# Kernel optimization log

Hardware: AMD Instinct MI355X
Metric: run time of the kernel (lower is better)

## Reference

```python
import jax, jax.numpy as jnp
import numpy as np

B, H = 65536, 256  # batch, hidden_size (== input_size since combine = input + hidden)


def setup_inputs() -> dict:
    key = jax.random.key(0)
    ks = jax.random.split(key, 11)
    s = 1.0 / np.sqrt(H)  # nn.Linear default init scale
    return {
        "input": jax.random.normal(ks[0], (B, H), jnp.float32),
        "hidden": jax.random.normal(ks[1], (B, H), jnp.float32),
        "cell": jax.random.normal(ks[2], (B, H), jnp.float32),
        "Wf": jax.random.uniform(ks[3], (H, H), jnp.float32, -s, s),
        "bf": jax.random.uniform(ks[4], (H,), jnp.float32, -s, s),
        "Wc": jax.random.uniform(ks[5], (H, H), jnp.float32, -s, s),
        "bc": jax.random.uniform(ks[6], (H,), jnp.float32, -s, s),
        "Wi": jax.random.uniform(ks[7], (H, H), jnp.float32, -s, s),
        "bi": jax.random.uniform(ks[8], (H,), jnp.float32, -s, s),
        "Wo": jax.random.uniform(ks[9], (H, H), jnp.float32, -s, s),
        "bo": jax.random.uniform(ks[10], (H,), jnp.float32, -s, s),
    }


def reference(input, hidden, cell, Wf, bf, Wc, bc, Wi, bi, Wo, bo):
    combine = input + hidden                                   # [B, H]
    ft = jax.nn.sigmoid(combine @ Wf.T + bf)                   # forget gate
    ct_ = jnp.tanh(combine @ Wc.T + bc)                        # candidate
    it = jax.nn.sigmoid(jax.nn.sigmoid(combine @ Wi.T + bi))   # note: double sigmoid, as in source
    cell_state = cell * ft + ct_ * it                          # [B, H]
    out = jax.nn.sigmoid(combine @ Wo.T + bo)                  # output gate
    hidden_state = out * jnp.tanh(cell_state)
    return (out, hidden_state, cell_state)
```

## Files before the change

kernel.cpp:

```cpp
#include <hip/hip_runtime.h>
#include <hip/hip_bf16.h>


typedef __attribute__((ext_vector_type(8))) short short8;
typedef __attribute__((ext_vector_type(4))) float f32x4;

static constexpr int Bsz   = 65536;
static constexpr int Hdim  = 256;
static constexpr int TROWS = 64;
static constexpr int NBLK  = (Bsz / TROWS) * 2;

__device__ __forceinline__ short f2bf(float f) {
    unsigned u = __float_as_uint(f);
    return (short)((u + 0x7FFFu + ((u >> 16) & 1u)) >> 16);
}
__device__ __forceinline__ float fast_rcp(float x) {
    float r;
    asm("v_rcp_f32 %0, %1" : "=v"(r) : "v"(x));
    return r;
}
__device__ __forceinline__ float sigm(float x) {
    return fast_rcp(1.0f + __expf(-x));
}
__device__ __forceinline__ float tanh_fast(float x) {
    return 2.0f * fast_rcp(1.0f + __expf(-2.0f * x)) - 1.0f;
}

__global__ void __launch_bounds__(256)
prep_w_kernel(const float* __restrict__ Wf, const float* __restrict__ Wc,
              const float* __restrict__ Wi, const float* __restrict__ Wo,
              short* __restrict__ Bp)
{
    int o    = blockIdx.x * 256 + threadIdx.x;
    int e    = o & 7;
    int lane = (o >> 3) & 63;
    int jf   = (o >> 9) & 15;
    int ks   = (o >> 13) & 7;
    int g    = (o >> 16) & 3;
    int k = ks * 32 + (lane >> 4) * 8 + e;
    int j = jf * 16 + (lane & 15);
    const float* W = (g == 0) ? Wf : (g == 1) ? Wc : (g == 2) ? Wi : Wo;
    Bp[o] = f2bf(W[j * 256 + k]);
}

__global__ void __launch_bounds__(512, 4)
lstm_main(const float* __restrict__ inp, const float* __restrict__ hid,
          const float* __restrict__ cell, const short* __restrict__ Bp,
          const float* __restrict__ bfv, const float* __restrict__ bcv,
          const float* __restrict__ biv, const float* __restrict__ bov,
          float* __restrict__ out)
{
    __shared__ short As[TROWS * Hdim];

    const int tid  = threadIdx.x;
    const int lane = tid & 63;
    const int wave = tid >> 6;
    const int lm   = lane & 15;
    const int lk   = lane >> 4;

    const int bid     = blockIdx.x;
    const int rowtile = (bid >> 4) * 8 + (bid & 7);
    const int jh      = (bid >> 3) & 1;
    const int rowblk  = rowtile * TROWS;

    const int j         = jh * 128 + wave * 16 + lm;
    const int jf_global = jh * 8 + wave;

#pragma unroll
    for (int round = 0; round < 2; ++round) {
        float4 Li[2][2], Lh[2][2];
#pragma unroll
        for (int c = 0; c < 2; ++c) {
            int cc  = tid + (round * 2 + c) * 512;
            int row = cc >> 5;
            int k0  = (cc & 31) * 8;
            const float4* ip = reinterpret_cast<const float4*>(inp + (size_t)(rowblk + row) * Hdim + k0);
            const float4* hp = reinterpret_cast<const float4*>(hid + (size_t)(rowblk + row) * Hdim + k0);
            Li[c][0] = ip[0]; Li[c][1] = ip[1];
            Lh[c][0] = hp[0]; Lh[c][1] = hp[1];
        }
#pragma unroll
        for (int c = 0; c < 2; ++c) {
            int cc  = tid + (round * 2 + c) * 512;
            int row = cc >> 5;
            int k0  = (cc & 31) * 8;
            short8 v;
            v[0] = f2bf(Li[c][0].x + Lh[c][0].x);
            v[1] = f2bf(Li[c][0].y + Lh[c][0].y);
            v[2] = f2bf(Li[c][0].z + Lh[c][0].z);
            v[3] = f2bf(Li[c][0].w + Lh[c][0].w);
            v[4] = f2bf(Li[c][1].x + Lh[c][1].x);
            v[5] = f2bf(Li[c][1].y + Lh[c][1].y);
            v[6] = f2bf(Li[c][1].z + Lh[c][1].z);
            v[7] = f2bf(Li[c][1].w + Lh[c][1].w);
            int byte = (row * 512 + k0 * 2) ^ ((row & 7) << 4);
            *reinterpret_cast<short8*>(reinterpret_cast<char*>(As) + byte) = v;
        }
    }

    const float bF = bfv[j], bC = bcv[j], bI = biv[j], bO = bov[j];

    __syncthreads();

    f32x4 acc[4][4];
    acc[0][0] = (f32x4){bF, bF, bF, bF};
    acc[1][0] = (f32x4){bC, bC, bC, bC};
    acc[2][0] = (f32x4){bI, bI, bI, bI};
    acc[3][0] = (f32x4){bO, bO, bO, bO};
#pragma unroll
    for (int g = 0; g < 4; ++g)
#pragma unroll
        for (int mf = 1; mf < 4; ++mf)
            acc[g][mf] = acc[g][0];

    const char* A = reinterpret_cast<const char*>(As);
#pragma unroll
    for (int ks = 0; ks < 8; ++ks) {
        short8 cf[4];
#pragma unroll
        for (int mf = 0; mf < 4; ++mf) {
            int row  = mf * 16 + lm;
            int byte = (row * 512 + (ks * 32 + lk * 8) * 2) ^ ((row & 7) << 4);
            cf[mf] = *reinterpret_cast<const short8*>(A + byte);
        }
#pragma unroll
        for (int g = 0; g < 4; ++g) {
            int chunk = (g * 8 + ks) * 16 + jf_global;
            short8 b = *reinterpret_cast<const short8*>(
                           Bp + ((size_t)chunk * 64 + lane) * 8);
            acc[g][0] = __builtin_amdgcn_mfma_f32_16x16x32_bf16(cf[0], b, acc[g][0], 0, 0, 0);
            acc[g][1] = __builtin_amdgcn_mfma_f32_16x16x32_bf16(cf[1], b, acc[g][1], 0, 0, 0);
            acc[g][2] = __builtin_amdgcn_mfma_f32_16x16x32_bf16(cf[2], b, acc[g][2], 0, 0, 0);
            acc[g][3] = __builtin_amdgcn_mfma_f32_16x16x32_bf16(cf[3], b, acc[g][3], 0, 0, 0);
        }
    }

    float* out0 = out;
    float* out1 = out + (size_t)Bsz * Hdim;
    float* out2 = out + (size_t)2 * Bsz * Hdim;

#pragma unroll
    for (int mf = 0; mf < 4; ++mf) {
        float cv[4];
#pragma unroll
        for (int r = 0; r < 4; ++r)
            cv[r] = cell[(size_t)(rowblk + mf * 16 + lk * 4 + r) * Hdim + j];
#pragma unroll
        for (int r = 0; r < 4; ++r) {
            int row = rowblk + mf * 16 + lk * 4 + r;
            size_t off = (size_t)row * Hdim + j;
            float F = sigm(acc[0][mf][r]);
            float C = tanh_fast(acc[1][mf][r]);
            float I = sigm(sigm(acc[2][mf][r]));
            float O = sigm(acc[3][mf][r]);
            float cs = cv[r] * F + C * I;
            float hs = O * tanh_fast(cs);
            out0[off] = O;
            out1[off] = hs;
            out2[off] = cs;
        }
    }
}

extern "C" void kernel_launch(void* const* d_in, const int* in_sizes, int n_in,
                              void* d_out, int out_size, void* d_ws, size_t ws_size,
                              hipStream_t stream)
{
    const float* inp  = (const float*)d_in[0];
    const float* hid  = (const float*)d_in[1];
    const float* cell = (const float*)d_in[2];
    const float* Wf   = (const float*)d_in[3];
    const float* bf_  = (const float*)d_in[4];
    const float* Wc   = (const float*)d_in[5];
    const float* bc_  = (const float*)d_in[6];
    const float* Wi   = (const float*)d_in[7];
    const float* bi_  = (const float*)d_in[8];
    const float* Wo   = (const float*)d_in[9];
    const float* bo_  = (const float*)d_in[10];

    short* Bp = (short*)d_ws;

    prep_w_kernel<<<1024, 256, 0, stream>>>(Wf, Wc, Wi, Wo, Bp);
    lstm_main<<<NBLK, 512, 0, stream>>>(inp, hid, cell, Bp,
                                        bf_, bc_, bi_, bo_, (float*)d_out);
}
```

Baseline: 116.2 us.

## Process two row tiles per block, prefetching second tile during first MFMA loop

Each block now handles two 64-row tiles using a double-buffered LDS staging area. Loads of the second tile's input and hidden rows are issued before the first tile's MFMA k-loop, so global-load latency overlaps with compute. The grid is halved and the occupancy hint drops from 4 to 2 blocks per CU. LDS use doubles and more registers hold the prefetched data, which may lower occupancy.

```diff
diff --git a/kernel.cpp b/kernel.cpp
--- a/kernel.cpp
+++ b/kernel.cpp
@@ -8,7 +8,7 @@
 static constexpr int Bsz   = 65536;
 static constexpr int Hdim  = 256;
 static constexpr int TROWS = 64;
-static constexpr int NBLK  = (Bsz / TROWS) * 2;
+static constexpr int NBLK  = (Bsz / (TROWS * 2)) * 2;
 
 __device__ __forceinline__ short f2bf(float f) {
     unsigned u = __float_as_uint(f);
@@ -43,14 +43,14 @@
     Bp[o] = f2bf(W[j * 256 + k]);
 }
 
-__global__ void __launch_bounds__(512, 4)
+__global__ void __launch_bounds__(512, 2)
 lstm_main(const float* __restrict__ inp, const float* __restrict__ hid,
           const float* __restrict__ cell, const short* __restrict__ Bp,
           const float* __restrict__ bfv, const float* __restrict__ bcv,
           const float* __restrict__ biv, const float* __restrict__ bov,
           float* __restrict__ out)
 {
-    __shared__ short As[TROWS * Hdim];
+    __shared__ short As[2][TROWS * Hdim];
 
     const int tid  = threadIdx.x;
     const int lane = tid & 63;
@@ -59,31 +59,34 @@
     const int lk   = lane >> 4;
 
     const int bid     = blockIdx.x;
-    const int rowtile = (bid >> 4) * 8 + (bid & 7);
+    const int rowpair = (bid >> 4) * 8 + (bid & 7);
     const int jh      = (bid >> 3) & 1;
-    const int rowblk  = rowtile * TROWS;
+    const int rowblk  = rowpair * (TROWS * 2);
 
     const int j         = jh * 128 + wave * 16 + lm;
     const int jf_global = jh * 8 + wave;
 
-#pragma unroll
-    for (int round = 0; round < 2; ++round) {
-        float4 Li[2][2], Lh[2][2];
-#pragma unroll
-        for (int c = 0; c < 2; ++c) {
-            int cc  = tid + (round * 2 + c) * 512;
-            int row = cc >> 5;
-            int k0  = (cc & 31) * 8;
-            const float4* ip = reinterpret_cast<const float4*>(inp + (size_t)(rowblk + row) * Hdim + k0);
-            const float4* hp = reinterpret_cast<const float4*>(hid + (size_t)(rowblk + row) * Hdim + k0);
+    const int s_row = tid >> 5;
+    const int s_k0  = (tid & 31) * 8;
+
+    float4 Li[4][2], Lh[4][2];
+
+    auto issue = [&](int t) {
+#pragma unroll
+        for (int c = 0; c < 4; ++c) {
+            int row = s_row + c * 16;
+            const float4* ip = reinterpret_cast<const float4*>(
+                inp + (size_t)(rowblk + t * TROWS + row) * Hdim + s_k0);
+            const float4* hp = reinterpret_cast<const float4*>(
+                hid + (size_t)(rowblk + t * TROWS + row) * Hdim + s_k0);
             Li[c][0] = ip[0]; Li[c][1] = ip[1];
             Lh[c][0] = hp[0]; Lh[c][1] = hp[1];
         }
-#pragma unroll
-        for (int c = 0; c < 2; ++c) {
-            int cc  = tid + (round * 2 + c) * 512;
-            int row = cc >> 5;
-            int k0  = (cc & 31) * 8;
+    };
+    auto writeb = [&](int buf) {
+#pragma unroll
+        for (int c = 0; c < 4; ++c) {
+            int row = s_row + c * 16;
             short8 v;
             v[0] = f2bf(Li[c][0].x + Lh[c][0].x);
             v[1] = f2bf(Li[c][0].y + Lh[c][0].y);
@@ -93,73 +96,93 @@
             v[5] = f2bf(Li[c][1].y + Lh[c][1].y);
             v[6] = f2bf(Li[c][1].z + Lh[c][1].z);
             v[7] = f2bf(Li[c][1].w + Lh[c][1].w);
-            int byte = (row * 512 + k0 * 2) ^ ((row & 7) << 4);
-            *reinterpret_cast<short8*>(reinterpret_cast<char*>(As) + byte) = v;
-        }
-    }
+            int byte = (row * 512 + s_k0 * 2) ^ ((row & 7) << 4);
+            *reinterpret_cast<short8*>(
+                reinterpret_cast<char*>(As[buf]) + byte) = v;
+        }
+    };
 
     const float bF = bfv[j], bC = bcv[j], bI = biv[j], bO = bov[j];
 
-    __syncthreads();
-
-    f32x4 acc[4][4];
-    acc[0][0] = (f32x4){bF, bF, bF, bF};
-    acc[1][0] = (f32x4){bC, bC, bC, bC};
-    acc[2][0] = (f32x4){bI, bI, bI, bI};
-    acc[3][0] = (f32x4){bO, bO, bO, bO};
-#pragma unroll
-    for (int g = 0; g < 4; ++g)
-#pragma unroll
-        for (int mf = 1; mf < 4; ++mf)
-            acc[g][mf] = acc[g][0];
-
-    const char* A = reinterpret_cast<const char*>(As);
-#pragma unroll
-    for (int ks = 0; ks < 8; ++ks) {
-        short8 cf[4];
-#pragma unroll
-        for (int mf = 0; mf < 4; ++mf) {
-            int row  = mf * 16 + lm;
-            int byte = (row * 512 + (ks * 32 + lk * 8) * 2) ^ ((row & 7) << 4);
-            cf[mf] = *reinterpret_cast<const short8*>(A + byte);
-        }
-#pragma unroll
-        for (int g = 0; g < 4; ++g) {
-            int chunk = (g * 8 + ks) * 16 + jf_global;
-            short8 b = *reinterpret_cast<const short8*>(
-                           Bp + ((size_t)chunk * 64 + lane) * 8);
-            acc[g][0] = __builtin_amdgcn_mfma_f32_16x16x32_bf16(cf[0], b, acc[g][0], 0, 0, 0);
-            acc[g][1] = __builtin_amdgcn_mfma_f32_16x16x32_bf16(cf[1], b, acc[g][1], 0, 0, 0);
-            acc[g][2] = __builtin_amdgcn_mfma_f32_16x16x32_bf16(cf[2], b, acc[g][2], 0, 0, 0);
-            acc[g][3] = __builtin_amdgcn_mfma_f32_16x16x32_bf16(cf[3], b, acc[g][3], 0, 0, 0);
-        }
-    }
+    auto kloop = [&](const short* Abuf, f32x4 (&acc)[4][4]) {
+        acc[0][0] = (f32x4){bF, bF, bF, bF};
+        acc[1][0] = (f32x4){bC, bC, bC, bC};
+        acc[2][0] = (f32x4){bI, bI, bI, bI};
+        acc[3][0] = (f32x4){bO, bO, bO, bO};
+#pragma unroll
+        for (int g = 0; g < 4; ++g)
+#pragma unroll
+            for (int mf = 1; mf < 4; ++mf)
+                acc[g][mf] = acc[g][0];
+        const char* A = reinterpret_cast<const char*>(Abuf);
+#pragma unroll
+        for (int ks = 0; ks < 8; ++ks) {
+            short8 cf[4];
+#pragma unroll
+            for (int mf = 0; mf < 4; ++mf) {
+                int row  = mf * 16 + lm;
+                int byte = (row * 512 + (ks * 32 + lk * 8) * 2) ^ ((row & 7) << 4);
+                cf[mf] = *reinterpret_cast<const short8*>(A + byte);
+            }
+#pragma unroll
+            for (int g = 0; g < 4; ++g) {
+                int chunk = (g * 8 + ks) * 16 + jf_global;
+                short8 b = *reinterpret_cast<const short8*>(
+                               Bp + ((size_t)chunk * 64 + lane) * 8);
+                acc[g][0] = __builtin_amdgcn_mfma_f32_16x16x32_bf16(cf[0], b, acc[g][0], 0, 0, 0);
+                acc[g][1] = __builtin_amdgcn_mfma_f32_16x16x32_bf16(cf[1], b, acc[g][1], 0, 0, 0);
+                acc[g][2] = __builtin_amdgcn_mfma_f32_16x16x32_bf16(cf[2], b, acc[g][2], 0, 0, 0);
+                acc[g][3] = __builtin_amdgcn_mfma_f32_16x16x32_bf16(cf[3], b, acc[g][3], 0, 0, 0);
+            }
+        }
+    };
 
     float* out0 = out;
     float* out1 = out + (size_t)Bsz * Hdim;
     float* out2 = out + (size_t)2 * Bsz * Hdim;
 
-#pragma unroll
-    for (int mf = 0; mf < 4; ++mf) {
-        float cv[4];
-#pragma unroll
-        for (int r = 0; r < 4; ++r)
-            cv[r] = cell[(size_t)(rowblk + mf * 16 + lk * 4 + r) * Hdim + j];
-#pragma unroll
-        for (int r = 0; r < 4; ++r) {
-            int row = rowblk + mf * 16 + lk * 4 + r;
-            size_t off = (size_t)row * Hdim + j;
-            float F = sigm(acc[0][mf][r]);
-            float C = tanh_fast(acc[1][mf][r]);
-            float I = sigm(sigm(acc[2][mf][r]));
-            float O = sigm(acc[3][mf][r]);
-            float cs = cv[r] * F + C * I;
-            float hs = O * tanh_fast(cs);
-            out0[off] = O;
-            out1[off] = hs;
-            out2[off] = cs;
-        }
-    }
+    auto epilogue = [&](int t, f32x4 (&acc)[4][4]) {
+        const int r0 = rowblk + t * TROWS;
+#pragma unroll
+        for (int mf = 0; mf < 4; ++mf) {
+            float cv[4];
+#pragma unroll
+            for (int r = 0; r < 4; ++r)
+                cv[r] = cell[(size_t)(r0 + mf * 16 + lk * 4 + r) * Hdim + j];
+#pragma unroll
+            for (int r = 0; r < 4; ++r) {
+                int row = r0 + mf * 16 + lk * 4 + r;
+                size_t off = (size_t)row * Hdim + j;
+                float F = sigm(acc[0][mf][r]);
+                float C = tanh_fast(acc[1][mf][r]);
+                float I = sigm(sigm(acc[2][mf][r]));
+                float O = sigm(acc[3][mf][r]);
+                float cs = cv[r] * F + C * I;
+                float hs = O * tanh_fast(cs);
+                out0[off] = O;
+                out1[off] = hs;
+                out2[off] = cs;
+            }
+        }
+    };
+
+    issue(0);
+    asm volatile("" ::: "memory");
+    writeb(0);
+    __syncthreads();
+
+    issue(1);
+    asm volatile("" ::: "memory");
+
+    f32x4 acc[4][4];
+    kloop(As[0], acc);
+
+    writeb(1);
+    __syncthreads();
+
+    epilogue(0, acc);
+    kloop(As[1], acc);
+    epilogue(1, acc);
 }
 
 extern "C" void kernel_launch(void* const* d_in, const int* in_sizes, int n_in,
```

New measurement: 152.5 us. 31.2% more time.

## Process two row tiles per block, overlapping next tile loads with epilogue

Applied to the files above, without the earlier changes.

Each block now handles two 64-row tiles with double-buffered LDS, which halves the grid size. Global loads of input and hidden for the second tile are issued before the first tile's epilogue, so memory latency is hidden behind the activation math and stores. The cost is doubled LDS per block (64KB), which may reduce occupancy, plus higher register pressure from keeping loads in flight during the epilogue.

```diff
diff --git a/kernel.cpp b/kernel.cpp
--- a/kernel.cpp
+++ b/kernel.cpp
@@ -8,7 +8,7 @@
 static constexpr int Bsz   = 65536;
 static constexpr int Hdim  = 256;
 static constexpr int TROWS = 64;
-static constexpr int NBLK  = (Bsz / TROWS) * 2;
+static constexpr int NBLK  = (Bsz / (TROWS * 2)) * 2;
 
 __device__ __forceinline__ short f2bf(float f) {
     unsigned u = __float_as_uint(f);
@@ -50,7 +50,7 @@
           const float* __restrict__ biv, const float* __restrict__ bov,
           float* __restrict__ out)
 {
-    __shared__ short As[TROWS * Hdim];
+    __shared__ short As[2][TROWS * Hdim];
 
     const int tid  = threadIdx.x;
     const int lane = tid & 63;
@@ -59,26 +59,36 @@
     const int lk   = lane >> 4;
 
     const int bid     = blockIdx.x;
-    const int rowtile = (bid >> 4) * 8 + (bid & 7);
+    const int rowpair = (bid >> 4) * 8 + (bid & 7);
     const int jh      = (bid >> 3) & 1;
-    const int rowblk  = rowtile * TROWS;
+    const int rowblk  = rowpair * (TROWS * 2);
 
     const int j         = jh * 128 + wave * 16 + lm;
     const int jf_global = jh * 8 + wave;
 
-#pragma unroll
-    for (int round = 0; round < 2; ++round) {
-        float4 Li[2][2], Lh[2][2];
+    float* out0 = out;
+    float* out1 = out + (size_t)Bsz * Hdim;
+    float* out2 = out + (size_t)2 * Bsz * Hdim;
+
+    const float bF = bfv[j], bC = bcv[j], bI = biv[j], bO = bov[j];
+
+    f32x4 acc[4][4];
+
+    auto issue_round = [&](int t, int round, float4 (&Li)[2][2], float4 (&Lh)[2][2]) {
 #pragma unroll
         for (int c = 0; c < 2; ++c) {
             int cc  = tid + (round * 2 + c) * 512;
             int row = cc >> 5;
             int k0  = (cc & 31) * 8;
-            const float4* ip = reinterpret_cast<const float4*>(inp + (size_t)(rowblk + row) * Hdim + k0);
-            const float4* hp = reinterpret_cast<const float4*>(hid + (size_t)(rowblk + row) * Hdim + k0);
+            const float4* ip = reinterpret_cast<const float4*>(
+                inp + (size_t)(rowblk + t * TROWS + row) * Hdim + k0);
+            const float4* hp = reinterpret_cast<const float4*>(
+                hid + (size_t)(rowblk + t * TROWS + row) * Hdim + k0);
             Li[c][0] = ip[0]; Li[c][1] = ip[1];
             Lh[c][0] = hp[0]; Lh[c][1] = hp[1];
         }
+    };
+    auto write_round = [&](int buf, int round, float4 (&Li)[2][2], float4 (&Lh)[2][2]) {
 #pragma unroll
         for (int c = 0; c < 2; ++c) {
             int cc  = tid + (round * 2 + c) * 512;
@@ -94,72 +104,96 @@
             v[6] = f2bf(Li[c][1].z + Lh[c][1].z);
             v[7] = f2bf(Li[c][1].w + Lh[c][1].w);
             int byte = (row * 512 + k0 * 2) ^ ((row & 7) << 4);
-            *reinterpret_cast<short8*>(reinterpret_cast<char*>(As) + byte) = v;
+            *reinterpret_cast<short8*>(
+                reinterpret_cast<char*>(As[buf]) + byte) = v;
+        }
+    };
+    auto kloop = [&](int buf) {
+        acc[0][0] = (f32x4){bF, bF, bF, bF};
+        acc[1][0] = (f32x4){bC, bC, bC, bC};
+        acc[2][0] = (f32x4){bI, bI, bI, bI};
+        acc[3][0] = (f32x4){bO, bO, bO, bO};
+#pragma unroll
+        for (int g = 0; g < 4; ++g)
+#pragma unroll
+            for (int mf = 1; mf < 4; ++mf)
+                acc[g][mf] = acc[g][0];
+        const char* A = reinterpret_cast<const char*>(As[buf]);
+#pragma unroll
+        for (int ks = 0; ks < 8; ++ks) {
+            short8 cf[4];
+#pragma unroll
+            for (int mf = 0; mf < 4; ++mf) {
+                int row  = mf * 16 + lm;
+                int byte = (row * 512 + (ks * 32 + lk * 8) * 2) ^ ((row & 7) << 4);
+                cf[mf] = *reinterpret_cast<const short8*>(A + byte);
+            }
+#pragma unroll
+            for (int g = 0; g < 4; ++g) {
+                int chunk = (g * 8 + ks) * 16 + jf_global;
+                short8 b = *reinterpret_cast<const short8*>(
+                               Bp + ((size_t)chunk * 64 + lane) * 8);
+                acc[g][0] = __builtin_amdgcn_mfma_f32_16x16x32_bf16(cf[0], b, acc[g][0], 0, 0, 0);
+                acc[g][1] = __builtin_amdgcn_mfma_f32_16x16x32_bf16(cf[1], b, acc[g][1], 0, 0, 0);
+                acc[g][2] = __builtin_amdgcn_mfma_f32_16x16x32_bf16(cf[2], b, acc[g][2], 0, 0, 0);
+                acc[g][3] = __builtin_amdgcn_mfma_f32_16x16x32_bf16(cf[3], b, acc[g][3], 0, 0, 0);
+            }
+        }
+    };
+    auto epi_half = [&](int t, int h) {
+        const int r0 = rowblk + t * TROWS;
+#pragma unroll
+        for (int m = 0; m < 2; ++m) {
+            const int mf = h * 2 + m;
+            float cv[4];
+#pragma unroll
+            for (int r = 0; r < 4; ++r)
+                cv[r] = cell[(size_t)(r0 + mf * 16 + lk * 4 + r) * Hdim + j];
+#pragma unroll
+            for (int r = 0; r < 4; ++r) {
+                int row = r0 + mf * 16 + lk * 4 + r;
+                size_t off = (size_t)row * Hdim + j;
+                float F = sigm(acc[0][mf][r]);
+                float C = tanh_fast(acc[1][mf][r]);
+                float I = sigm(sigm(acc[2][mf][r]));
+                float O = sigm(acc[3][mf][r]);
+                float cs = cv[r] * F + C * I;
+                float hs = O * tanh_fast(cs);
+                out0[off] = O;
+                out1[off] = hs;
+                out2[off] = cs;
+            }
+        }
+    };
+
+    {
+        float4 Li[2][2], Lh[2][2];
+#pragma unroll
+        for (int round = 0; round < 2; ++round) {
+            issue_round(0, round, Li, Lh);
+            write_round(0, round, Li, Lh);
         }
     }
-
-    const float bF = bfv[j], bC = bcv[j], bI = biv[j], bO = bov[j];
-
     __syncthreads();
 
-    f32x4 acc[4][4];
-    acc[0][0] = (f32x4){bF, bF, bF, bF};
-    acc[1][0] = (f32x4){bC, bC, bC, bC};
-    acc[2][0] = (f32x4){bI, bI, bI, bI};
-    acc[3][0] = (f32x4){bO, bO, bO, bO};
-#pragma unroll
-    for (int g = 0; g < 4; ++g)
-#pragma unroll
-        for (int mf = 1; mf < 4; ++mf)
-            acc[g][mf] = acc[g][0];
-
-    const char* A = reinterpret_cast<const char*>(As);
-#pragma unroll
-    for (int ks = 0; ks < 8; ++ks) {
-        short8 cf[4];
-#pragma unroll
-        for (int mf = 0; mf < 4; ++mf) {
-            int row  = mf * 16 + lm;
-            int byte = (row * 512 + (ks * 32 + lk * 8) * 2) ^ ((row & 7) << 4);
-            cf[mf] = *reinterpret_cast<const short8*>(A + byte);
-        }
-#pragma unroll
-        for (int g = 0; g < 4; ++g) {
-            int chunk = (g * 8 + ks) * 16 + jf_global;
-            short8 b = *reinterpret_cast<const short8*>(
-                           Bp + ((size_t)chunk * 64 + lane) * 8);
-            acc[g][0] = __builtin_amdgcn_mfma_f32_16x16x32_bf16(cf[0], b, acc[g][0], 0, 0, 0);
-            acc[g][1] = __builtin_amdgcn_mfma_f32_16x16x32_bf16(cf[1], b, acc[g][1], 0, 0, 0);
-            acc[g][2] = __builtin_amdgcn_mfma_f32_16x16x32_bf16(cf[2], b, acc[g][2], 0, 0, 0);
-            acc[g][3] = __builtin_amdgcn_mfma_f32_16x16x32_bf16(cf[3], b, acc[g][3], 0, 0, 0);
-        }
+    kloop(0);
+
+    {
+        float4 Li[2][2], Lh[2][2];
+        issue_round(1, 0, Li, Lh);
+        asm volatile("" ::: "memory");
+        epi_half(0, 0);
+        write_round(1, 0, Li, Lh);
+        issue_round(1, 1, Li, Lh);
+        asm volatile("" ::: "memory");
+        epi_half(0, 1);
+        write_round(1, 1, Li, Lh);
     }
-
-    float* out0 = out;
-    float* out1 = out + (size_t)Bsz * Hdim;
-    float* out2 = out + (size_t)2 * Bsz * Hdim;
-
-#pragma unroll
-    for (int mf = 0; mf < 4; ++mf) {
-        float cv[4];
-#pragma unroll
-        for (int r = 0; r < 4; ++r)
-            cv[r] = cell[(size_t)(rowblk + mf * 16 + lk * 4 + r) * Hdim + j];
-#pragma unroll
-        for (int r = 0; r < 4; ++r) {
-            int row = rowblk + mf * 16 + lk * 4 + r;
-            size_t off = (size_t)row * Hdim + j;
-            float F = sigm(acc[0][mf][r]);
-            float C = tanh_fast(acc[1][mf][r]);
-            float I = sigm(sigm(acc[2][mf][r]));
-            float O = sigm(acc[3][mf][r]);
-            float cs = cv[r] * F + C * I;
-            float hs = O * tanh_fast(cs);
-            out0[off] = O;
-            out1[off] = hs;
-            out2[off] = cs;
-        }
-    }
+    __syncthreads();
+
+    kloop(1);
+    epi_half(1, 0);
+    epi_half(1, 1);
 }
 
 extern "C" void kernel_launch(void* const* d_in, const int* in_sizes, int n_in,
```

Result: slower. 227.9 us (+96.1%).
